# Performance work log

Hardware: AMD Instinct MI355X
Metric: run time of the kernel (lower is better)

The kernel has to match this reference:

```python
import jax, jax.numpy as jnp
import numpy as np

DIM = 128
HID = 1024
B = 1024


def _mlp(x, W1, b1, W2, b2, W3, b3):
    h = jnp.tanh(x @ W1 + b1)
    h = jnp.tanh(h @ W2 + b2)
    return h @ W3 + b3


def setup_inputs() -> dict:
    key = jax.random.key(0)
    ks = jax.random.split(key, 8)

    def w(k, shape):
        return (jax.random.normal(k, shape, jnp.float32) / np.float32(np.sqrt(shape[0])))

    # states = [mu | sigma_diag]; sigma_diag must be positive (it is a variance)
    states = jax.random.uniform(ks[0], (B, 2 * DIM), jnp.float32) + jnp.float32(0.05)
    t = jnp.float32(0.25)
    inp = dict(states=states, t=t)
    # dynamics_net params (input = dim + 1 for time)
    inp["dW1"] = w(ks[1], (DIM + 1, HID)); inp["db1"] = jnp.zeros((HID,), jnp.float32)
    inp["dW2"] = w(ks[2], (HID, HID));     inp["db2"] = jnp.zeros((HID,), jnp.float32)
    inp["dW3"] = w(ks[3], (HID, DIM));     inp["db3"] = jnp.zeros((DIM,), jnp.float32)
    # noise_net params (diagonal Q via softplus)
    inp["nW1"] = w(ks[4], (DIM + 1, HID)); inp["nb1"] = jnp.zeros((HID,), jnp.float32)
    inp["nW2"] = w(ks[5], (HID, HID));     inp["nb2"] = jnp.zeros((HID,), jnp.float32)
    inp["nW3"] = w(ks[6], (HID, DIM));     inp["nb3"] = jnp.zeros((DIM,), jnp.float32)
    return inp


def reference(states, t, dW1, db1, dW2, db2, dW3, db3, nW1, nb1, nW2, nb2, nW3, nb3):
    dim = DIM
    mu = states[:, :dim]          # [B, dim]
    sigma = states[:, dim:]       # [B, dim] diagonal covariance
    tcol = jnp.full((mu.shape[0], 1), t, mu.dtype)

    # drift of the mean (batched MLP)
    mu_drift = _mlp(jnp.concatenate([mu, tcol], axis=1), dW1, db1, dW2, db2, dW3, db3)

    # diagonal of the Jacobian d mu_drift / d mu, per sample.
    # The torch code loops over dim doing one autograd.grad per row; here one
    # vmapped jacfwd collapses that into a single batched forward-mode pass.
    def dyn_single(mu_s):  # [dim] -> [dim]
        x = jnp.concatenate([mu_s, jnp.reshape(t, (1,))])
        return _mlp(x, dW1, db1, dW2, db2, dW3, db3)

    J = jax.vmap(jax.jacfwd(dyn_single))(mu)          # [B, dim, dim]
    J_diag = jnp.diagonal(J, axis1=1, axis2=2)         # [B, dim]

    # process noise: diagonal of Q (softplus for PSD)
    q_raw = _mlp(jnp.concatenate([mu, tcol], axis=1), nW1, nb1, nW2, nb2, nW3, nb3)
    Q_diag = jax.nn.softplus(q_raw)                    # [B, dim]

    sigma_drift = 2.0 * J_diag * sigma + Q_diag
    log_density_drift = -jnp.sum(J_diag, axis=1) + 0.5 * jnp.sum(
        Q_diag / (sigma + 1e-6), axis=1
    )
    return jnp.concatenate([mu_drift, sigma_drift], axis=1), log_density_drift
```

## Files before the change

kernel.cpp:

```cpp
#include <hip/hip_runtime.h>
#include <math.h>

typedef unsigned short u16;
typedef unsigned int u32;
typedef __bf16 bf16x8 __attribute__((ext_vector_type(8)));
typedef float f32x4 __attribute__((ext_vector_type(4)));

#define NB 1024
#define HID 1024

__device__ __forceinline__ float bfu(u16 u) { return __uint_as_float(((u32)u) << 16); }
__device__ __forceinline__ u16 f2bf(float f) {
    u32 u = __float_as_uint(f);
    return (u16)((u + 0x7fffu + ((u >> 16) & 1u)) >> 16);
}
__device__ __forceinline__ u32 mulbf2(u32 a, u32 b) {
    float a0 = __uint_as_float(a << 16), a1 = __uint_as_float(a & 0xffff0000u);
    float b0 = __uint_as_float(b << 16), b1 = __uint_as_float(b & 0xffff0000u);
    u32 u0 = __float_as_uint(a0 * b0), u1 = __float_as_uint(a1 * b1);
    return ((u0 + 0x8000u) >> 16) | ((u1 + 0x8000u) & 0xffff0000u);
}

#if __has_builtin(__builtin_amdgcn_global_load_lds)
#define HAVE_GLL 1
#else
#define HAVE_GLL 0
#endif

__device__ __forceinline__ void stage16(const void* g, void* ldsbase, int lane) {
#if HAVE_GLL
    typedef const __attribute__((address_space(1))) unsigned char ga_t;
    typedef __attribute__((address_space(3))) unsigned char la_t;
    __builtin_amdgcn_global_load_lds((ga_t*)(unsigned long long)g,
                                     (la_t*)(u32)(unsigned long long)ldsbase,
                                     16, 0, 0);
#else
    *reinterpret_cast<uint4*>((char*)ldsbase + lane * 16) =
        *reinterpret_cast<const uint4*>(g);
#endif
}

#define SBAR __builtin_amdgcn_sched_barrier(0)


__device__ __forceinline__ void stage_tile(const u16* src, int ld, u16* dst, int tid) {
    int w = tid >> 6, lane = tid & 63;
#pragma unroll
    for (int q = 0; q < 4; ++q) {
        int rbase = q * 32 + w * 8;
        int row = rbase + (lane >> 3);
        stage16(src + (size_t)row * ld + (lane & 7) * 8, dst + rbase * 64, lane);
    }
}

__device__ __forceinline__ void mfma_block(const u16* As, const u16* Bs,
                                           f32x4 acc[4][4], int wr, int wc, int lane) {
    int lr = lane >> 4, lc = lane & 15;
#pragma unroll
    for (int kc = 0; kc < 64; kc += 32) {
        bf16x8 av[4], bv[4];
#pragma unroll
        for (int it = 0; it < 4; ++it)
            av[it] = *(const bf16x8*)&As[(wr * 64 + it * 16 + lc) * 64 + kc + lr * 8];
#pragma unroll
        for (int nt = 0; nt < 4; ++nt)
            bv[nt] = *(const bf16x8*)&Bs[(wc * 64 + nt * 16 + lc) * 64 + kc + lr * 8];
#pragma unroll
        for (int it = 0; it < 4; ++it)
#pragma unroll
            for (int nt = 0; nt < 4; ++nt)
                acc[it][nt] = __builtin_amdgcn_mfma_f32_16x16x32_bf16(
                    av[it], bv[nt], acc[it][nt], 0, 0, 0);
    }
}


__global__ __launch_bounds__(256) void k_cast(const float* in, u16* out, int n) {
    int i = blockIdx.x * 256 + threadIdx.x;
    if (i < n) out[i] = f2bf(in[i]);
}

__global__ __launch_bounds__(256) void k_transposeB(const float* inA, const float* inB,
                                                    u16* outA, u16* outB, int R, int C) {
    const float* in = blockIdx.z ? inB : inA;
    u16* out = blockIdx.z ? outB : outA;
    __shared__ u16 tile[32][33];
    int c0 = blockIdx.x * 32, r0 = blockIdx.y * 32;
    int tx = threadIdx.x, ty = threadIdx.y;
#pragma unroll
    for (int dy = 0; dy < 32; dy += 8)
        tile[ty + dy][tx] = f2bf(in[(size_t)(r0 + ty + dy) * C + c0 + tx]);
    __syncthreads();
#pragma unroll
    for (int dy = 0; dy < 32; dy += 8)
        out[(size_t)(c0 + ty + dy) * R + r0 + tx] = tile[tx][ty + dy];
}

__global__ __launch_bounds__(256) void k_layer1(const float* states, const float* tptr,
                                                const float* dW1, const float* db1,
                                                const float* nW1, const float* nb1,
                                                u16* h1d, u16* h1n, u16* g1d) {
    __shared__ float xt[129][8];
    int blk = blockIdx.x, q = blockIdx.y, net = blockIdx.z, tid = threadIdx.x;
    float t = *tptr;
    for (int idx = tid; idx < 8 * 128; idx += 256) {
        int d = idx >> 3, s = idx & 7;
        xt[d][s] = states[(size_t)(blk * 8 + s) * 256 + d];
    }
    if (tid < 8) xt[128][tid] = t;
    __syncthreads();
    const float* W = net ? nW1 : dW1;
    const float* bi = net ? nb1 : db1;
    u16* H = net ? h1n : h1d;
    int o = q * 256 + tid;
    float acc[8] = {0.f, 0.f, 0.f, 0.f, 0.f, 0.f, 0.f, 0.f};
    for (int d = 0; d < 129; ++d) {
        float w = W[(size_t)d * 1024 + o];
        float4 xa = *(const float4*)&xt[d][0];
        float4 xb = *(const float4*)&xt[d][4];
        acc[0] += xa.x * w; acc[1] += xa.y * w; acc[2] += xa.z * w; acc[3] += xa.w * w;
        acc[4] += xb.x * w; acc[5] += xb.y * w; acc[6] += xb.z * w; acc[7] += xb.w * w;
    }
    float b = bi[o];
#pragma unroll
    for (int s = 0; s < 8; ++s) {
        float h = tanhf(acc[s] + b);
        H[(size_t)(blk * 8 + s) * 1024 + o] = f2bf(h);
        if (!net) g1d[(size_t)(blk * 8 + s) * 1024 + o] = f2bf(1.f - h * h);
    }
}

__global__ __launch_bounds__(256) void k_l2part(const u16* Ad, const u16* An,
                                                const u16* Wd, const u16* Wn,
                                                float* P) {
    int x = blockIdx.x;
    int nt = x & 7, ks = x >> 3;
    int mt = blockIdx.y, net = blockIdx.z;
    const u16* A = net ? An : Ad;
    const u16* W = net ? Wn : Wd;
    int n0 = nt * 128, row0 = mt * 128;
    int kbeg = ks * 512;
    __shared__ __align__(16) u16 As[128 * 64], Bs[128 * 64];
    int tid = threadIdx.x, w = tid >> 6, lane = tid & 63;
    int wr = w >> 1, wc = w & 1, lr = lane >> 4, lc = lane & 15;
    f32x4 acc[4][4];
#pragma unroll
    for (int a = 0; a < 4; ++a)
#pragma unroll
        for (int b2 = 0; b2 < 4; ++b2) { f32x4 zz = {0.f, 0.f, 0.f, 0.f}; acc[a][b2] = zz; }
    for (int k0 = kbeg; k0 < kbeg + 512; k0 += 64) {
        stage_tile(A + (size_t)row0 * 1024 + k0, 1024, As, tid);
        stage_tile(W + (size_t)n0 * 1024 + k0, 1024, Bs, tid);
        __syncthreads();
        mfma_block(As, Bs, acc, wr, wc, lane);
        __syncthreads();
    }
    float* dst = P + (size_t)(net * 2 + ks) * 1024 * 1024;
#pragma unroll
    for (int it = 0; it < 4; ++it)
#pragma unroll
        for (int nt2 = 0; nt2 < 4; ++nt2) {
            int col = n0 + wc * 64 + nt2 * 16 + lc;
#pragma unroll
            for (int r = 0; r < 4; ++r) {
                int row = row0 + wr * 64 + it * 16 + lr * 4 + r;
                dst[(size_t)row * 1024 + col] = acc[it][nt2][r];
            }
        }
}

__global__ __launch_bounds__(256) void k_h2fin(const float* P, const float* db2,
                                               const float* nb2, u16* h2d, u16* h2n) {
    int net = blockIdx.y;
    const float* b = net ? nb2 : db2;
    u16* H = net ? h2n : h2d;
    size_t idx = (size_t)blockIdx.x * 256 + threadIdx.x;
    int col = (int)(idx & 1023);
    const float* P0 = P + (size_t)(net * 2) * 1024 * 1024;
    const float* P1 = P + (size_t)(net * 2 + 1) * 1024 * 1024;
    H[idx] = f2bf(tanhf(P0[idx] + P1[idx] + b[col]));
}

__global__ __launch_bounds__(256) void k_l3part(const u16* Ad, const u16* An,
                                                const u16* Wd, const u16* Wn,
                                                float* P) {
    int ks = blockIdx.x, mt = blockIdx.y, net = blockIdx.z;
    const u16* A = net ? An : Ad;
    const u16* W = net ? Wn : Wd;
    int row0 = mt * 128, kbeg = ks * 256;
    __shared__ __align__(16) u16 As[128 * 64], Bs[128 * 64];
    int tid = threadIdx.x, w = tid >> 6, lane = tid & 63;
    int wr = w >> 1, wc = w & 1, lr = lane >> 4, lc = lane & 15;
    f32x4 acc[4][4];
#pragma unroll
    for (int a = 0; a < 4; ++a)
#pragma unroll
        for (int b2 = 0; b2 < 4; ++b2) { f32x4 zz = {0.f, 0.f, 0.f, 0.f}; acc[a][b2] = zz; }
    for (int k0 = kbeg; k0 < kbeg + 256; k0 += 64) {
        stage_tile(A + (size_t)row0 * 1024 + k0, 1024, As, tid);
        stage_tile(W + (size_t)k0, 1024, Bs, tid);
        __syncthreads();
        mfma_block(As, Bs, acc, wr, wc, lane);
        __syncthreads();
    }
    float* dst = P + (size_t)(net * 4 + ks) * 1024 * 128;
#pragma unroll
    for (int it = 0; it < 4; ++it)
#pragma unroll
        for (int nt2 = 0; nt2 < 4; ++nt2) {
            int col = wc * 64 + nt2 * 16 + lc;
#pragma unroll
            for (int r = 0; r < 4; ++r) {
                int row = row0 + wr * 64 + it * 16 + lr * 4 + r;
                dst[(size_t)row * 128 + col] = acc[it][nt2][r];
            }
        }
}


__global__ __launch_bounds__(512, 4) void k_jacf(const u16* dW1bf, const u16* g1d,
                                                 const u16* W2T, const u16* W3T,
                                                 const u16* h2d, float* Jpart) {
    __shared__ __align__(16) u16 smA[2][128 * 32];
    __shared__ __align__(16) u16 smB[2][256 * 32];
    int tid = threadIdx.x, lane = tid & 63, w = tid >> 6;
    int wr = w >> 2, wc = w & 3, lr = lane >> 4, lc = lane & 15;
    int hID = blockIdx.x;
    int lin = (hID & 7) * 512 + (hID >> 3);
    int mt = lin >> 2, nt = lin & 3;
    int n0 = nt * 256;
    const u16* Bp = W2T + (size_t)n0 * 1024;
    const u16* grow = g1d + (size_t)mt * 1024;

    f32x4 acc[4][4];
#pragma unroll
    for (int m = 0; m < 4; ++m)
#pragma unroll
        for (int n = 0; n < 4; ++n) { f32x4 zz = {0.f, 0.f, 0.f, 0.f}; acc[m][n] = zz; }

    int ar_ = tid >> 2, ac_ = tid & 3;
    int asw = ac_ ^ ((ar_ >> 1) & 3);
    uint4 wv, gv;

    auto issueA = [&](int k0) {
        wv = *(const uint4*)&dW1bf[(size_t)ar_ * 1024 + k0 + asw * 8];
        gv = *(const uint4*)&grow[k0 + asw * 8];
    };
    auto writeA = [&](u16* dst) {
        uint4 o;
        o.x = mulbf2(wv.x, gv.x);
        o.y = mulbf2(wv.y, gv.y);
        o.z = mulbf2(wv.z, gv.z);
        o.w = mulbf2(wv.w, gv.w);
        *(uint4*)&dst[ar_ * 32 + ac_ * 8] = o;
    };
    auto stageB = [&](int k0, u16* dst) {
#pragma unroll
        for (int q = 0; q < 2; ++q) {
            int cid = q * 512 + tid;
            int r = cid >> 2, c = cid & 3;
            stage16(Bp + (size_t)r * 1024 + k0 + ((c ^ ((r >> 1) & 3)) << 3),
                    dst + (q * 512 + w * 64) * 8, lane);
        }
    };
    auto compute = [&](const u16* As_, const u16* Bs_) {
        bf16x8 av[4], bv[4];
#pragma unroll
        for (int m = 0; m < 4; ++m) {
            int row = wr * 64 + m * 16 + lc;
            av[m] = *(const bf16x8*)&As_[row * 32 + ((lr ^ ((row >> 1) & 3)) << 3)];
        }
#pragma unroll
        for (int n = 0; n < 4; ++n) {
            int row = wc * 64 + n * 16 + lc;
            bv[n] = *(const bf16x8*)&Bs_[row * 32 + ((lr ^ ((row >> 1) & 3)) << 3)];
        }
        __builtin_amdgcn_s_setprio(1);
#pragma unroll
        for (int m = 0; m < 4; ++m)
#pragma unroll
            for (int n = 0; n < 4; ++n)
                acc[m][n] = __builtin_amdgcn_mfma_f32_16x16x32_bf16(
                    av[m], bv[n], acc[m][n], 0, 0, 0);
        __builtin_amdgcn_s_setprio(0);
    };

    issueA(0);
    stageB(0, smB[0]);
    writeA(smA[0]);
    __syncthreads();

    for (int t = 0; t < 32; ++t) {
        int p = t & 1;
        if (t < 31) {
            issueA((t + 1) * 32);
            stageB((t + 1) * 32, smB[p ^ 1]);
        }
        SBAR;
        compute(smA[p], smB[p]);
        if (t < 31) writeA(smA[p ^ 1]);
        __syncthreads();
    }

    float g2v[4];
#pragma unroll
    for (int n = 0; n < 4; ++n) {
        int k2 = n0 + wc * 64 + n * 16 + lc;
        float h2 = bfu(h2d[(size_t)mt * 1024 + k2]);
        g2v[n] = 1.f - h2 * h2;
    }
    float* jtmp = (float*)&smA[0][0];
#pragma unroll
    for (int m = 0; m < 4; ++m) {
#pragma unroll
        for (int r = 0; r < 4; ++r) {
            int i = wr * 64 + m * 16 + lr * 4 + r;
            float p = 0.f;
#pragma unroll
            for (int n = 0; n < 4; ++n) {
                int k2 = n0 + wc * 64 + n * 16 + lc;
                float w3 = bfu(W3T[(size_t)i * 1024 + k2]);
                p += acc[m][n][r] * g2v[n] * w3;
            }
#pragma unroll
            for (int msk = 1; msk < 16; msk <<= 1) p += __shfl_xor(p, msk, 64);
            if (lc == 0) jtmp[wc * 128 + i] = p;
        }
    }
    __syncthreads();
    if (tid < 128) {
        float s = jtmp[tid] + jtmp[128 + tid] + jtmp[256 + tid] + jtmp[384 + tid];
        Jpart[((size_t)mt * 4 + nt) * 128 + tid] = s;
    }
}

__global__ __launch_bounds__(128) void k_final(const float* states, const float* Jpart,
                                               const float* L3part, const float* db3,
                                               const float* nb3, float* out) {
    int b = blockIdx.x, i = threadIdx.x;
    float jd = 0.f;
#pragma unroll
    for (int kb = 0; kb < 4; ++kb) jd += Jpart[((size_t)b * 4 + kb) * 128 + i];
    float mu = db3[i], qr = nb3[i];
#pragma unroll
    for (int ks = 0; ks < 4; ++ks) {
        mu += L3part[((size_t)(0 * 4 + ks) * 1024 + b) * 128 + i];
        qr += L3part[((size_t)(1 * 4 + ks) * 1024 + b) * 128 + i];
    }
    out[(size_t)b * 256 + i] = mu;
    float q = (qr > 20.f) ? qr : log1pf(expf(qr));
    float sig = states[(size_t)b * 256 + 128 + i];
    out[(size_t)b * 256 + 128 + i] = 2.f * jd * sig + q;
    float s1 = jd;
    float s2 = q / (sig + 1e-6f);
#pragma unroll
    for (int m = 32; m >= 1; m >>= 1) {
        s1 += __shfl_down(s1, m, 64);
        s2 += __shfl_down(s2, m, 64);
    }
    __shared__ float red[4];
    int wv = i >> 6, ln = i & 63;
    if (ln == 0) { red[wv * 2] = s1; red[wv * 2 + 1] = s2; }
    __syncthreads();
    if (i == 0) out[(size_t)NB * 256 + b] = -(red[0] + red[2]) + 0.5f * (red[1] + red[3]);
}

extern "C" void kernel_launch(void* const* d_in, const int* in_sizes, int n_in,
                              void* d_out, int out_size, void* d_ws, size_t ws_size,
                              hipStream_t stream) {
    (void)in_sizes; (void)n_in; (void)out_size; (void)ws_size;
    const float* states = (const float*)d_in[0];
    const float* tptr   = (const float*)d_in[1];
    const float* dW1 = (const float*)d_in[2];  const float* db1 = (const float*)d_in[3];
    const float* dW2 = (const float*)d_in[4];  const float* db2 = (const float*)d_in[5];
    const float* dW3 = (const float*)d_in[6];  const float* db3 = (const float*)d_in[7];
    const float* nW1 = (const float*)d_in[8];  const float* nb1 = (const float*)d_in[9];
    const float* nW2 = (const float*)d_in[10]; const float* nb2 = (const float*)d_in[11];
    const float* nW3 = (const float*)d_in[12]; const float* nb3 = (const float*)d_in[13];
    float* out = (float*)d_out;
    char* ws = (char*)d_ws;

    u16* dW1bf = (u16*)(ws + 0);
    u16* dW2T  = (u16*)(ws + 262144);
    u16* nW2T  = (u16*)(ws + 2359296);
    u16* dW3T  = (u16*)(ws + 4456448);
    u16* nW3T  = (u16*)(ws + 4718592);
    u16* h1d   = (u16*)(ws + 4980736);
    u16* h1n   = (u16*)(ws + 7077888);
    u16* h2d   = (u16*)(ws + 9175040);
    u16* h2n   = (u16*)(ws + 11272192);
    u16* g1d   = (u16*)(ws + 13369344);
    float* Jpart  = (float*)(ws + 15466496);
    float* L3part = (float*)(ws + 17563648);
    float* H2part = (float*)(ws + 21757952);

    k_cast<<<512, 256, 0, stream>>>(dW1, dW1bf, 128 * 1024);
    dim3 tb(32, 8);
    k_transposeB<<<dim3(32, 32, 2), tb, 0, stream>>>(dW2, nW2, dW2T, nW2T, 1024, 1024);
    k_transposeB<<<dim3(4, 32, 2), tb, 0, stream>>>(dW3, nW3, dW3T, nW3T, 1024, 128);
    k_layer1<<<dim3(128, 4, 2), 256, 0, stream>>>(states, tptr, dW1, db1, nW1, nb1,
                                                  h1d, h1n, g1d);
    k_l2part<<<dim3(16, 8, 2), 256, 0, stream>>>(h1d, h1n, dW2T, nW2T, H2part);
    k_h2fin<<<dim3(4096, 2), 256, 0, stream>>>(H2part, db2, nb2, h2d, h2n);
    k_l3part<<<dim3(4, 8, 2), 256, 0, stream>>>(h2d, h2n, dW3T, nW3T, L3part);
    k_jacf<<<4096, 512, 0, stream>>>(dW1bf, g1d, dW2T, dW3T, h2d, Jpart);
    k_final<<<1024, 128, 0, stream>>>(states, Jpart, L3part, db3, nb3, out);
}
```

Before: 381.7 us.

## Double k-tile depth in Jacobian GEMM, single-buffer scaled A tile

Measured after the change: 347.6 us. 8.9% less time.

```diff
diff --git a/kernel.cpp b/kernel.cpp
--- a/kernel.cpp
+++ b/kernel.cpp
@@ -14,11 +14,13 @@
     u32 u = __float_as_uint(f);
     return (u16)((u + 0x7fffu + ((u >> 16) & 1u)) >> 16);
 }
-__device__ __forceinline__ u32 mulbf2(u32 a, u32 b) {
-    float a0 = __uint_as_float(a << 16), a1 = __uint_as_float(a & 0xffff0000u);
-    float b0 = __uint_as_float(b << 16), b1 = __uint_as_float(b & 0xffff0000u);
-    u32 u0 = __float_as_uint(a0 * b0), u1 = __float_as_uint(a1 * b1);
-    return ((u0 + 0x8000u) >> 16) | ((u1 + 0x8000u) & 0xffff0000u);
+
+__device__ __forceinline__ uint4 scale8(uint4 wv, uint4 gv) {
+    union U { uint4 u; __bf16 h[8]; } a, g, r;
+    a.u = wv; g.u = gv;
+#pragma unroll
+    for (int e = 0; e < 8; ++e) r.h[e] = (__bf16)((float)a.h[e] * (float)g.h[e]);
+    return r.u;
 }
 
 #if __has_builtin(__builtin_amdgcn_global_load_lds)
@@ -41,6 +43,7 @@
 }
 
 #define SBAR __builtin_amdgcn_sched_barrier(0)
+#define WBAR __builtin_amdgcn_s_barrier()
 
 
 __device__ __forceinline__ void stage_tile(const u16* src, int ld, u16* dst, int tid) {
@@ -221,16 +224,22 @@
 __global__ __launch_bounds__(512, 4) void k_jacf(const u16* dW1bf, const u16* g1d,
                                                  const u16* W2T, const u16* W3T,
                                                  const u16* h2d, float* Jpart) {
-    __shared__ __align__(16) u16 smA[2][128 * 32];
-    __shared__ __align__(16) u16 smB[2][256 * 32];
+    __shared__ __align__(16) u16 smA[128 * 64];
+    __shared__ __align__(16) u16 smB[2][256 * 64];
     int tid = threadIdx.x, lane = tid & 63, w = tid >> 6;
     int wr = w >> 2, wc = w & 3, lr = lane >> 4, lc = lane & 15;
     int hID = blockIdx.x;
     int lin = (hID & 7) * 512 + (hID >> 3);
     int mt = lin >> 2, nt = lin & 3;
     int n0 = nt * 256;
-    const u16* Bp = W2T + (size_t)n0 * 1024;
-    const u16* grow = g1d + (size_t)mt * 1024;
+
+    int r0 = tid >> 3, c0 = tid & 7;
+    int csw = (c0 ^ (r0 & 7)) * 8;
+    const u16* aptr = dW1bf + (size_t)r0 * 1024 + csw;
+    const u16* gptr = g1d + (size_t)mt * 1024 + csw;
+    const u16* bptr = W2T + (size_t)(n0 + r0) * 1024 + csw;
+    int d0 = r0 * 64 + c0 * 8;
+    int d1 = d0 + 4096;
 
     f32x4 acc[4][4];
 #pragma unroll
@@ -238,67 +247,63 @@
 #pragma unroll
         for (int n = 0; n < 4; ++n) { f32x4 zz = {0.f, 0.f, 0.f, 0.f}; acc[m][n] = zz; }
 
-    int ar_ = tid >> 2, ac_ = tid & 3;
-    int asw = ac_ ^ ((ar_ >> 1) & 3);
-    uint4 wv, gv;
-
-    auto issueA = [&](int k0) {
-        wv = *(const uint4*)&dW1bf[(size_t)ar_ * 1024 + k0 + asw * 8];
-        gv = *(const uint4*)&grow[k0 + asw * 8];
-    };
-    auto writeA = [&](u16* dst) {
-        uint4 o;
-        o.x = mulbf2(wv.x, gv.x);
-        o.y = mulbf2(wv.y, gv.y);
-        o.z = mulbf2(wv.z, gv.z);
-        o.w = mulbf2(wv.w, gv.w);
-        *(uint4*)&dst[ar_ * 32 + ac_ * 8] = o;
-    };
-    auto stageB = [&](int k0, u16* dst) {
-#pragma unroll
-        for (int q = 0; q < 2; ++q) {
-            int cid = q * 512 + tid;
-            int r = cid >> 2, c = cid & 3;
-            stage16(Bp + (size_t)r * 1024 + k0 + ((c ^ ((r >> 1) & 3)) << 3),
-                    dst + (q * 512 + w * 64) * 8, lane);
-        }
-    };
-    auto compute = [&](const u16* As_, const u16* Bs_) {
-        bf16x8 av[4], bv[4];
-#pragma unroll
-        for (int m = 0; m < 4; ++m) {
-            int row = wr * 64 + m * 16 + lc;
-            av[m] = *(const bf16x8*)&As_[row * 32 + ((lr ^ ((row >> 1) & 3)) << 3)];
-        }
-#pragma unroll
-        for (int n = 0; n < 4; ++n) {
-            int row = wc * 64 + n * 16 + lc;
-            bv[n] = *(const bf16x8*)&Bs_[row * 32 + ((lr ^ ((row >> 1) & 3)) << 3)];
-        }
-        __builtin_amdgcn_s_setprio(1);
-#pragma unroll
-        for (int m = 0; m < 4; ++m)
-#pragma unroll
-            for (int n = 0; n < 4; ++n)
-                acc[m][n] = __builtin_amdgcn_mfma_f32_16x16x32_bf16(
-                    av[m], bv[n], acc[m][n], 0, 0, 0);
-        __builtin_amdgcn_s_setprio(0);
-    };
-
-    issueA(0);
-    stageB(0, smB[0]);
-    writeA(smA[0]);
+    int colr = (lr ^ (lc & 7)) * 8;
+
+    {
+        uint4 gv = *(const uint4*)gptr;
+        uint4 wv0 = *(const uint4*)aptr;
+        uint4 wv1 = *(const uint4*)(aptr + 65536);
+#pragma unroll
+        for (int q = 0; q < 4; ++q)
+            stage16(bptr + q * 65536, smB[0] + (q * 512 + w * 64) * 8, lane);
+        aptr += 64; gptr += 64; bptr += 64;
+        uint4 s0 = scale8(wv0, gv), s1 = scale8(wv1, gv);
+        *(uint4*)&smA[d0] = s0;
+        *(uint4*)&smA[d1] = s1;
+    }
     __syncthreads();
 
-    for (int t = 0; t < 32; ++t) {
+    for (int t = 0; t < 16; ++t) {
         int p = t & 1;
-        if (t < 31) {
-            issueA((t + 1) * 32);
-            stageB((t + 1) * 32, smB[p ^ 1]);
+        uint4 wv0, wv1, gv;
+        if (t < 15) {
+            gv = *(const uint4*)gptr;
+            wv0 = *(const uint4*)aptr;
+            wv1 = *(const uint4*)(aptr + 65536);
+#pragma unroll
+            for (int q = 0; q < 4; ++q)
+                stage16(bptr + q * 65536, smB[p ^ 1] + (q * 512 + w * 64) * 8, lane);
+            aptr += 64; gptr += 64; bptr += 64;
         }
         SBAR;
-        compute(smA[p], smB[p]);
-        if (t < 31) writeA(smA[p ^ 1]);
+        {
+            const u16* Bs_ = smB[p];
+            __builtin_amdgcn_s_setprio(1);
+#pragma unroll
+            for (int kh = 0; kh < 2; ++kh) {
+                int col = colr ^ (kh * 32);
+                bf16x8 av[4], bv[4];
+#pragma unroll
+                for (int m = 0; m < 4; ++m)
+                    av[m] = *(const bf16x8*)&smA[(wr * 64 + m * 16 + lc) * 64 + col];
+#pragma unroll
+                for (int n = 0; n < 4; ++n)
+                    bv[n] = *(const bf16x8*)&Bs_[(wc * 64 + n * 16 + lc) * 64 + col];
+#pragma unroll
+                for (int m = 0; m < 4; ++m)
+#pragma unroll
+                    for (int n = 0; n < 4; ++n)
+                        acc[m][n] = __builtin_amdgcn_mfma_f32_16x16x32_bf16(
+                            av[m], bv[n], acc[m][n], 0, 0, 0);
+            }
+            __builtin_amdgcn_s_setprio(0);
+        }
+        SBAR; WBAR; SBAR;
+        if (t < 15) {
+            uint4 s0 = scale8(wv0, gv), s1 = scale8(wv1, gv);
+            *(uint4*)&smA[d0] = s0;
+            *(uint4*)&smA[d1] = s1;
+        }
         __syncthreads();
     }
 
@@ -309,7 +314,7 @@
         float h2 = bfu(h2d[(size_t)mt * 1024 + k2]);
         g2v[n] = 1.f - h2 * h2;
     }
-    float* jtmp = (float*)&smA[0][0];
+    float* jtmp = (float*)&smA[0];
 #pragma unroll
     for (int m = 0; m < 4; ++m) {
 #pragma unroll
```
